# Optimization experiments

Hardware: AMD Instinct MI355X
Metric: run time of the kernel (lower is better)

Reference implementation:

```python
import jax, jax.numpy as jnp
import numpy as np

N = 50000       # nodes
E = 800000      # edges
IN_DIM = 256    # input_dim
HEADS = 4
CH = 32         # per-head channels (hidden_dim; conv3 uses latent_dim//heads = 32 too)
HC = HEADS * CH # 128
ED = 32         # edge_dims


def setup_inputs():
    key = jax.random.key(0)
    ks = iter(jax.random.split(key, 64))
    def nrm(shape):
        return jax.random.normal(next(ks), shape, dtype=jnp.float32) * 0.05
    inp = {}
    inp["x"] = nrm((N, IN_DIM))
    inp["edge_index"] = jax.random.randint(next(ks), (2, E), 0, N)
    inp["attr"] = nrm((E, ED))
    for l, ind in ((1, IN_DIM), (2, HC), (3, HC)):
        inp[f"Wq{l}"] = nrm((ind, HC)); inp[f"bq{l}"] = jnp.zeros((HC,), jnp.float32)
        inp[f"Wk{l}"] = nrm((ind, HC)); inp[f"bk{l}"] = jnp.zeros((HC,), jnp.float32)
        inp[f"Wv{l}"] = nrm((ind, HC)); inp[f"bv{l}"] = jnp.zeros((HC,), jnp.float32)
        inp[f"We{l}"] = nrm((ED, HC))  # lin_edge has no bias in PyG TransformerConv
        inp[f"Ws{l}"] = nrm((ind, HC)); inp[f"bs{l}"] = jnp.zeros((HC,), jnp.float32)
    inp["g1"] = jnp.ones((HC,), jnp.float32); inp["be1"] = jnp.zeros((HC,), jnp.float32)
    inp["g2"] = jnp.ones((HC,), jnp.float32); inp["be2"] = jnp.zeros((HC,), jnp.float32)
    return inp


def _transformer_conv(x, src, dst, attr, Wq, bq, Wk, bk, Wv, bv, We, Ws, bs):
    # PyG TransformerConv, concat=True, root_weight=True, beta=False, dropout=0 (eval).
    q = (x @ Wq + bq).reshape(-1, HEADS, CH)   # [N,H,C] (queries at dst)
    k = (x @ Wk + bk).reshape(-1, HEADS, CH)
    v = (x @ Wv + bv).reshape(-1, HEADS, CH)
    e = (attr @ We).reshape(-1, HEADS, CH)     # [E,H,C]
    kj = k[src] + e                            # edge-conditioned keys  [E,H,C]
    vj = v[src] + e                            # edge-conditioned values [E,H,C]
    alpha = jnp.einsum('ehc,ehc->eh', q[dst], kj) / np.sqrt(CH).astype(np.float32)
    # segment softmax over incoming edges per destination node, per head
    amax = jax.ops.segment_max(alpha, dst, num_segments=N)          # [N,H]
    amax = jnp.where(jnp.isfinite(amax), amax, 0.0)                 # nodes with no edges
    ex = jnp.exp(alpha - amax[dst])                                 # [E,H]
    den = jax.ops.segment_sum(ex, dst, num_segments=N)              # [N,H]
    a = ex / (den[dst] + 1e-16)                                     # [E,H]
    out = jax.ops.segment_sum(a[..., None] * vj, dst, num_segments=N)  # [N,H,C]
    out = out.reshape(-1, HC) + (x @ Ws + bs)                       # + root skip
    return out, a


def _layernorm(x, g, b):
    m = x.mean(-1, keepdims=True)
    v = x.var(-1, keepdims=True)
    return (x - m) / jnp.sqrt(v + 1e-5) * g + b


def reference(x, edge_index, attr,
              Wq1, bq1, Wk1, bk1, Wv1, bv1, We1, Ws1, bs1,
              Wq2, bq2, Wk2, bk2, Wv2, bv2, We2, Ws2, bs2,
              Wq3, bq3, Wk3, bk3, Wv3, bv3, We3, Ws3, bs3,
              g1, be1, g2, be2):
    src, dst = edge_index[0], edge_index[1]
    h, a1 = _transformer_conv(x, src, dst, attr, Wq1, bq1, Wk1, bk1, Wv1, bv1, We1, Ws1, bs1)
    h = jax.nn.relu(_layernorm(h, g1, be1))   # dropout is identity in eval
    h, a2 = _transformer_conv(h, src, dst, attr, Wq2, bq2, Wk2, bk2, Wv2, bv2, We2, Ws2, bs2)
    h = jax.nn.relu(_layernorm(h, g2, be2))
    h, a3 = _transformer_conv(h, src, dst, attr, Wq3, bq3, Wk3, bk3, Wv3, bv3, We3, Ws3, bs3)
    return (h, a1, a2, a3)
```

## Files before the change

### kernel.cpp

```cpp
#include <hip/hip_runtime.h>
#include <math.h>

#define N_NODES 50000
#define E_EDGES 800000
#define HC 128
#define ED 32
#define SCH 64
#define SCHSZ 782

typedef __attribute__((ext_vector_type(8))) short bf16x8;
typedef __attribute__((ext_vector_type(4))) float f32x4;
typedef unsigned short ushort_t;

__device__ __forceinline__ ushort_t f2bf(float f){
    unsigned u = __float_as_uint(f);
    return (ushort_t)((u + 0x7FFFu + ((u >> 16) & 1u)) >> 16);
}
__device__ __forceinline__ float bflo(unsigned u){ return __uint_as_float(u << 16); }
__device__ __forceinline__ float bfhi(unsigned u){ return __uint_as_float(u & 0xffff0000u); }

__device__ __forceinline__ int weidx(int c, int d){
    return c * 40 + (((((d >> 2) + ((c >> 3) & 7)) & 7)) << 2) + (d & 3);
}


__global__ void hist_kernel(const int* __restrict__ dst, int* __restrict__ cnt, int n_edges){
    int e = blockIdx.x * blockDim.x + threadIdx.x;
    if (e < n_edges) atomicAdd(&cnt[dst[e]], 1);
}

__global__ __launch_bounds__(256) void chunk_hist_kernel(const int* __restrict__ cnt,
                                                         int* __restrict__ chist,
                                                         int* __restrict__ csum){
    __shared__ int hist[64];
    __shared__ int red[256];
    const int t = threadIdx.x, b = blockIdx.x;
    if (t < 64) hist[t] = 0;
    __syncthreads();
    const int base = b * SCHSZ;
    const int lim = min(base + SCHSZ, N_NODES);
    int mysum = 0;
    for (int i = base + t; i < lim; i += 256){
        int d = cnt[i];
        mysum += d;
        if (d > 63) d = 63;
        atomicAdd(&hist[d], 1);
    }
    red[t] = mysum;
    __syncthreads();
    for (int off = 128; off; off >>= 1){
        if (t < off) red[t] += red[t + off];
        __syncthreads();
    }
    if (t < 64) chist[b * 64 + t] = hist[t];
    if (t == 0) csum[b] = red[0];
}

__global__ __launch_bounds__(256) void fill_rowptr_kernel(
    const int* __restrict__ cnt, const int* __restrict__ csum,
    int* __restrict__ rowptr, int* __restrict__ cursor)
{
    __shared__ int ts[256];
    __shared__ int chunkbase;
    const int b = blockIdx.x, t = threadIdx.x;
    if (t == 0){
        int acc = 0;
        for (int c = 0; c < b; c++) acc += csum[c];
        chunkbase = acc;
    }
    const int base = b * SCHSZ;
    const int lim = min(base + SCHSZ, N_NODES);
    const int idx0 = base + t * 4;
    int c[4];
    int local = 0;
    #pragma unroll
    for (int j = 0; j < 4; j++){
        int idx = idx0 + j;
        c[j] = (idx < lim) ? cnt[idx] : 0;
        local += c[j];
    }
    ts[t] = local;
    __syncthreads();
    for (int off = 1; off < 256; off <<= 1){
        int v = (t >= off) ? ts[t - off] : 0;
        __syncthreads();
        ts[t] += v;
        __syncthreads();
    }
    int off0 = chunkbase + ((t == 0) ? 0 : ts[t - 1]);
    #pragma unroll
    for (int j = 0; j < 4; j++){
        int idx = idx0 + j;
        if (idx < lim){
            rowptr[idx] = off0;
            cursor[idx] = off0;
            off0 += c[j];
        }
    }
    if (b == SCH - 1 && t == 255) rowptr[N_NODES] = chunkbase + ts[255];
}

__global__ __launch_bounds__(256) void scatter_kernel(
    const int* __restrict__ src, const int* __restrict__ dst,
    int* __restrict__ cursor, int2* __restrict__ es, int n_edges,
    const int* __restrict__ cnt, const int* __restrict__ chist, int* __restrict__ norder)
{
    __shared__ int chs[SCH * 64];
    __shared__ int bt[64];
    __shared__ int bb[64];
    __shared__ int cur[64];
    const int b = blockIdx.x, t = threadIdx.x;
    const bool sorter = (b < SCH);
    int pre = 0;
    if (sorter){
        for (int i = t; i < SCH * 64; i += 256) chs[i] = chist[i];
        __syncthreads();
        if (t < 64){
            int tot = 0;
            for (int c = 0; c < SCH; c++){
                int v = chs[c * 64 + t];
                tot += v;
                if (c < b) pre += v;
            }
            bt[t] = tot;
        }
        __syncthreads();
        if (t == 0){
            int a = 0;
            for (int d = 0; d < 64; d++){ int v = bt[d]; bb[d] = a; a += v; }
        }
        __syncthreads();
        if (t < 64) cur[t] = bb[t] + pre;
        __syncthreads();
    }
    int e = b * 256 + t;
    if (e < n_edges){
        int d = dst[e];
        int pos = atomicAdd(&cursor[d], 1);
        es[pos] = make_int2(e, src[e]);
    }
    if (sorter){
        const int base = b * SCHSZ;
        const int lim = min(base + SCHSZ, N_NODES);
        for (int i = base + t; i < lim; i += 256){
            int d = cnt[i]; if (d > 63) d = 63;
            int pos = atomicAdd(&cur[d], 1);
            norder[pos] = i;
        }
    }
}

__device__ __forceinline__ void pack_item(const float* __restrict__ Wq, const float* __restrict__ Wk,
                                          const float* __restrict__ Wv, const float* __restrict__ Ws,
                                          const float* __restrict__ We, ushort_t* __restrict__ Bp,
                                          int K, int item){
    int n = item % 640, k = item / 640;
    float val;
    if (n < 512){
        const float* W = (n < 128) ? Wq : (n < 256) ? Wk : (n < 384) ? Wv : Ws;
        val = W[k * HC + (n & 127)];
    } else {
        int col = n - 512, h5 = (col >> 5) * 32, d = col & 31;
        float acc = 0.f;
        for (int c = 0; c < 32; c++)
            acc = fmaf(Wq[k * HC + h5 + c], We[d * HC + h5 + c], acc);
        val = acc;
    }
    Bp[(((size_t)(k >> 3)) * 640 + n) * 8 + (k & 7)] = f2bf(val);
}

#define T_S0 12800000
#define T_S1 16000000
#define T_S2 16163840
#define T_S3 16245760
#define T_S4 16327680
#define T_S5 16328064

__global__ __launch_bounds__(256) void tail_kernel(
    const float* __restrict__ attr, const int2* __restrict__ es,
    const float* __restrict__ x, int perm_mode,
    ushort_t* __restrict__ attr_bf, ushort_t* __restrict__ Xbf,
    const float* __restrict__ Wq0, const float* __restrict__ bq0, const float* __restrict__ Wk0,
    const float* __restrict__ Wv0, const float* __restrict__ Ws0, const float* __restrict__ We0,
    const float* __restrict__ Wq1, const float* __restrict__ bq1, const float* __restrict__ Wk1,
    const float* __restrict__ Wv1, const float* __restrict__ Ws1, const float* __restrict__ We1,
    const float* __restrict__ Wq2, const float* __restrict__ bq2, const float* __restrict__ Wk2,
    const float* __restrict__ Wv2, const float* __restrict__ Ws2, const float* __restrict__ We2,
    ushort_t* __restrict__ Bp0, ushort_t* __restrict__ Bp1, ushort_t* __restrict__ Bp2,
    float* __restrict__ qwb3)
{
    const int stride = gridDim.x * blockDim.x;
    for (int gi = blockIdx.x * blockDim.x + threadIdx.x; gi < T_S5; gi += stride){
        if (gi < T_S0){
            if (perm_mode){
                int grp = gi >> 4, lane = gi & 15;
                int e = es[grp].x;
                const float2 v = *(const float2*)&attr[(size_t)e * ED + lane * 2];
                unsigned r = (unsigned)f2bf(v.x) | ((unsigned)f2bf(v.y) << 16);
                ((unsigned*)attr_bf)[(size_t)grp * (ED / 2) + lane] = r;
            }
        } else if (gi < T_S1){
            int i = gi - T_S0;
            float4 v = ((const float4*)x)[i];
            ushort_t r0 = f2bf(v.x), r1 = f2bf(v.y), r2 = f2bf(v.z), r3 = f2bf(v.w);
            ((ushort4*)Xbf)[i] = make_ushort4(r0, r1, r2, r3);
        } else if (gi < T_S2){
            pack_item(Wq0, Wk0, Wv0, Ws0, We0, Bp0, 256, gi - T_S1);
        } else if (gi < T_S3){
            pack_item(Wq1, Wk1, Wv1, Ws1, We1, Bp1, 128, gi - T_S2);
        } else if (gi < T_S4){
            pack_item(Wq2, Wk2, Wv2, Ws2, We2, Bp2, 128, gi - T_S3);
        } else {
            int f = gi - T_S4;
            int l = f >> 7, t2 = f & 127;
            const float* bq = (l == 0) ? bq0 : (l == 1) ? bq1 : bq2;
            const float* We = (l == 0) ? We0 : (l == 1) ? We1 : We2;
            int h5 = (t2 >> 5) * 32, d = t2 & 31;
            float acc = 0.f;
            for (int c = 0; c < 32; c++)
                acc = fmaf(bq[h5 + c], We[d * HC + h5 + c], acc);
            qwb3[l * HC + t2] = acc;
        }
    }
}

template<int K>
__global__ __launch_bounds__(320) void gemm_mfma(
    const ushort_t* __restrict__ Xbf, const ushort_t* __restrict__ Bpack,
    const float* __restrict__ b0, const float* __restrict__ b1,
    const float* __restrict__ b2, const float* __restrict__ b3,
    const float* __restrict__ b4,
    float* __restrict__ Yq, ushort_t* __restrict__ Ykbf,
    ushort_t* __restrict__ Yvbf, float* __restrict__ Ys,
    float* __restrict__ Yw, int M)
{
    const int w = threadIdx.x >> 6;
    const int lane = threadIdx.x & 63;
    const int q = lane >> 4, nn = lane & 15;
    const int row0 = blockIdx.x * 32;

    f32x4 acc[2][8];
    #pragma unroll
    for (int mt = 0; mt < 2; mt++)
        #pragma unroll
        for (int nt = 0; nt < 8; nt++)
            acc[mt][nt] = (f32x4){0.f, 0.f, 0.f, 0.f};

    const int r0 = row0 + nn;
    const int r1 = row0 + 16 + nn;
    const bf16x8 zf = (bf16x8){0,0,0,0,0,0,0,0};

    #pragma unroll
    for (int kc = 0; kc < K / 32; kc++){
        bf16x8 a0 = (r0 < M) ? *(const bf16x8*)&Xbf[(size_t)r0 * K + kc * 32 + q * 8] : zf;
        bf16x8 a1 = (r1 < M) ? *(const bf16x8*)&Xbf[(size_t)r1 * K + kc * 32 + q * 8] : zf;
        bf16x8 b[8];
        #pragma unroll
        for (int nt = 0; nt < 8; nt++){
            int n = w * 128 + nt * 16 + nn;
            b[nt] = *(const bf16x8*)&Bpack[(((size_t)(kc * 4 + q)) * 640 + n) * 8];
        }
        #pragma unroll
        for (int nt = 0; nt < 8; nt++){
            acc[0][nt] = __builtin_amdgcn_mfma_f32_16x16x32_bf16(a0, b[nt], acc[0][nt], 0, 0, 0);
            acc[1][nt] = __builtin_amdgcn_mfma_f32_16x16x32_bf16(a1, b[nt], acc[1][nt], 0, 0, 0);
        }
    }

    const float scale = (w == 0 || w == 4) ? 0.17677669529663687f : 1.f;
    const float* bias = (w == 0) ? b0 : (w == 1) ? b1 : (w == 2) ? b2 : (w == 3) ? b3 : b4;

    if (w == 1 || w == 2){
        ushort_t* Yb = (w == 1) ? Ykbf : Yvbf;
        #pragma unroll
        for (int nt = 0; nt < 8; nt++){
            int col = nt * 16 + nn;
            float bval = bias[col];
            #pragma unroll
            for (int mt = 0; mt < 2; mt++){
                #pragma unroll
                for (int r = 0; r < 4; r++){
                    int row = row0 + mt * 16 + q * 4 + r;
                    if (row < M) Yb[(size_t)row * HC + col] = f2bf(acc[mt][nt][r] + bval);
                }
            }
        }
    } else {
        float* Y = (w == 0) ? Yq : (w == 3) ? Ys : Yw;
        #pragma unroll
        for (int nt = 0; nt < 8; nt++){
            int col = nt * 16 + nn;
            float bval = bias[col];
            #pragma unroll
            for (int mt = 0; mt < 2; mt++){
                #pragma unroll
                for (int r = 0; r < 4; r++){
                    int row = row0 + mt * 16 + q * 4 + r;
                    if (row < M) Y[(size_t)row * HC + col] = (acc[mt][nt][r] + bval) * scale;
                }
            }
        }
    }
}

__device__ __forceinline__ float dot16s(const uint4 kk, const uint4 aa,
                                        const float4 qA, const float4 qB,
                                        const float4 wA, const float4 wB){
    float pa =            bflo(kk.x) * qA.x;
    pa = fmaf(bfhi(kk.x), qA.y, pa);
    pa = fmaf(bflo(kk.y), qA.z, pa);
    pa = fmaf(bfhi(kk.y), qA.w, pa);
    pa = fmaf(bflo(aa.x), wA.x, pa);
    pa = fmaf(bfhi(aa.x), wA.y, pa);
    pa = fmaf(bflo(aa.y), wA.z, pa);
    pa = fmaf(bfhi(aa.y), wA.w, pa);
    float pb =            bflo(kk.z) * qB.x;
    pb = fmaf(bfhi(kk.z), qB.y, pb);
    pb = fmaf(bflo(kk.w), qB.z, pb);
    pb = fmaf(bfhi(kk.w), qB.w, pb);
    pb = fmaf(bflo(aa.z), wB.x, pb);
    pb = fmaf(bfhi(aa.z), wB.y, pb);
    pb = fmaf(bflo(aa.w), wB.z, pb);
    pb = fmaf(bfhi(aa.w), wB.w, pb);
    return pa + pb;
}

__device__ __forceinline__ uint4 packrow(const float* p){
    float4 x = *(const float4*)p;
    float4 y = *(const float4*)(p + 4);
    uint4 r;
    r.x = (unsigned)f2bf(x.x) | ((unsigned)f2bf(x.y) << 16);
    r.y = (unsigned)f2bf(x.z) | ((unsigned)f2bf(x.w) << 16);
    r.z = (unsigned)f2bf(y.x) | ((unsigned)f2bf(y.y) << 16);
    r.w = (unsigned)f2bf(y.z) | ((unsigned)f2bf(y.w) << 16);
    return r;
}

__global__ __launch_bounds__(256) void fused_attn_kernel(
    const float* __restrict__ qs, const float* __restrict__ qw,
    const ushort_t* __restrict__ kb, const ushort_t* __restrict__ vb,
    const float* __restrict__ skip, const float* __restrict__ We,
    const float* __restrict__ attr, const ushort_t* __restrict__ attr_bf, int perm_mode,
    const int* __restrict__ rowptr, const int2* __restrict__ es,
    const int* __restrict__ norder,
    float* __restrict__ acsr, float* __restrict__ a_out,
    const float* __restrict__ g, const float* __restrict__ be,
    float* __restrict__ out_f32, ushort_t* __restrict__ out_bf, int apply_ln)
{
    __shared__ float WeT[5120];
    __shared__ float SL[2304];
    const int t = threadIdx.x;
    for (int idx = t; idx < ED * HC; idx += 256){
        int d = idx >> 7, c = idx & 127;
        WeT[weidx(c, d)] = We[idx];
    }
    __syncthreads();

    const int lane = t & 63, wvi = t >> 6;
    const int qq = lane >> 4, li = lane & 15;
    const int h = li >> 2, jj = li & 3;
    const int gq = blockIdx.x * 16 + wvi * 4 + qq;
    if (gq >= N_NODES) return;
    const int n = norder[gq];
    const int ch = h * 32 + jj * 8;
    const size_t nrow = (size_t)n * HC + ch;

    const float4 qA = *(const float4*)&qs[nrow];
    const float4 qB = *(const float4*)&qs[nrow + 4];
    const float4 wA = *(const float4*)&qw[nrow];
    const float4 wB = *(const float4*)&qw[nrow + 4];
    const float4 skA = *(const float4*)&skip[nrow];
    const float4 skB = *(const float4*)&skip[nrow + 4];

    const int beg = rowptr[n], end = rowptr[n + 1];
    float m = -1e30f, s = 0.f;
    float acc[8] = {0,0,0,0,0,0,0,0};
    float S[8]   = {0,0,0,0,0,0,0,0};

    for (int i = beg; i < end; i += 4){
        const int cnt = end - i;
        uint4 kk[4], vv[4], aa[4];
        #pragma unroll
        for (int b = 0; b < 4; b++){
            kk[b] = (uint4){0,0,0,0}; vv[b] = (uint4){0,0,0,0}; aa[b] = (uint4){0,0,0,0};
            if (b < cnt){
                const int2 e = es[i + b];
                kk[b] = *(const uint4*)&kb[(size_t)e.y * HC + ch];
                vv[b] = *(const uint4*)&vb[(size_t)e.y * HC + ch];
                if (perm_mode)
                    aa[b] = *(const uint4*)&attr_bf[(size_t)(i + b) * ED + jj * 8];
                else
                    aa[b] = packrow(&attr[(size_t)e.x * ED + jj * 8]);
            }
        }
        float al[4];
        #pragma unroll
        for (int b = 0; b < 4; b++){
            float p = dot16s(kk[b], aa[b], qA, qB, wA, wB);
            p += __shfl_xor(p, 1);
            p += __shfl_xor(p, 2);
            al[b] = (b < cnt) ? p : -1e38f;
        }
        if (jj == 0){
            #pragma unroll
            for (int b = 0; b < 4; b++)
                if (b < cnt) acsr[(size_t)(i + b) * 4 + h] = al[b];
        }
        const float mn = fmaxf(fmaxf(m, fmaxf(al[0], al[1])), fmaxf(al[2], al[3]));
        const float sc = __expf(m - mn);
        m = mn;
        const float w0 = __expf(al[0] - mn);
        const float w1 = __expf(al[1] - mn);
        const float w2 = __expf(al[2] - mn);
        const float w3 = __expf(al[3] - mn);
        s = fmaf(s, sc, (w0 + w1) + (w2 + w3));
        acc[0] = fmaf(acc[0], sc, fmaf(w0, bflo(vv[0].x), fmaf(w1, bflo(vv[1].x), fmaf(w2, bflo(vv[2].x), w3 * bflo(vv[3].x)))));
        acc[1] = fmaf(acc[1], sc, fmaf(w0, bfhi(vv[0].x), fmaf(w1, bfhi(vv[1].x), fmaf(w2, bfhi(vv[2].x), w3 * bfhi(vv[3].x)))));
        acc[2] = fmaf(acc[2], sc, fmaf(w0, bflo(vv[0].y), fmaf(w1, bflo(vv[1].y), fmaf(w2, bflo(vv[2].y), w3 * bflo(vv[3].y)))));
        acc[3] = fmaf(acc[3], sc, fmaf(w0, bfhi(vv[0].y), fmaf(w1, bfhi(vv[1].y), fmaf(w2, bfhi(vv[2].y), w3 * bfhi(vv[3].y)))));
        acc[4] = fmaf(acc[4], sc, fmaf(w0, bflo(vv[0].z), fmaf(w1, bflo(vv[1].z), fmaf(w2, bflo(vv[2].z), w3 * bflo(vv[3].z)))));
        acc[5] = fmaf(acc[5], sc, fmaf(w0, bfhi(vv[0].z), fmaf(w1, bfhi(vv[1].z), fmaf(w2, bfhi(vv[2].z), w3 * bfhi(vv[3].z)))));
        acc[6] = fmaf(acc[6], sc, fmaf(w0, bflo(vv[0].w), fmaf(w1, bflo(vv[1].w), fmaf(w2, bflo(vv[2].w), w3 * bflo(vv[3].w)))));
        acc[7] = fmaf(acc[7], sc, fmaf(w0, bfhi(vv[0].w), fmaf(w1, bfhi(vv[1].w), fmaf(w2, bfhi(vv[2].w), w3 * bfhi(vv[3].w)))));
        S[0] = fmaf(S[0], sc, fmaf(w0, bflo(aa[0].x), fmaf(w1, bflo(aa[1].x), fmaf(w2, bflo(aa[2].x), w3 * bflo(aa[3].x)))));
        S[1] = fmaf(S[1], sc, fmaf(w0, bfhi(aa[0].x), fmaf(w1, bfhi(aa[1].x), fmaf(w2, bfhi(aa[2].x), w3 * bfhi(aa[3].x)))));
        S[2] = fmaf(S[2], sc, fmaf(w0, bflo(aa[0].y), fmaf(w1, bflo(aa[1].y), fmaf(w2, bflo(aa[2].y), w3 * bflo(aa[3].y)))));
        S[3] = fmaf(S[3], sc, fmaf(w0, bfhi(aa[0].y), fmaf(w1, bfhi(aa[1].y), fmaf(w2, bfhi(aa[2].y), w3 * bfhi(aa[3].y)))));
        S[4] = fmaf(S[4], sc, fmaf(w0, bflo(aa[0].z), fmaf(w1, bflo(aa[1].z), fmaf(w2, bflo(aa[2].z), w3 * bflo(aa[3].z)))));
        S[5] = fmaf(S[5], sc, fmaf(w0, bfhi(aa[0].z), fmaf(w1, bfhi(aa[1].z), fmaf(w2, bfhi(aa[2].z), w3 * bfhi(aa[3].z)))));
        S[6] = fmaf(S[6], sc, fmaf(w0, bflo(aa[0].w), fmaf(w1, bflo(aa[1].w), fmaf(w2, bflo(aa[2].w), w3 * bflo(aa[3].w)))));
        S[7] = fmaf(S[7], sc, fmaf(w0, bfhi(aa[0].w), fmaf(w1, bfhi(aa[1].w), fmaf(w2, bfhi(aa[2].w), w3 * bfhi(aa[3].w)))));
    }

    const int nl = wvi * 4 + qq;
    const int sbase = nl * 144;
    const int hsk = h * 36;
    *(float4*)&SL[sbase + hsk + jj * 8]     = make_float4(S[0], S[1], S[2], S[3]);
    *(float4*)&SL[sbase + hsk + jj * 8 + 4] = make_float4(S[4], S[5], S[6], S[7]);
    asm volatile("" ::: "memory");
    float E[8] = {0,0,0,0,0,0,0,0};
    #pragma unroll
    for (int d4 = 0; d4 < 8; d4++){
        const float4 sv = *(const float4*)&SL[sbase + hsk + d4 * 4];
        #pragma unroll
        for (int r = 0; r < 8; r++){
            const float4 wv = *(const float4*)&WeT[weidx(ch + r, d4 * 4)];
            E[r] = fmaf(sv.x, wv.x, fmaf(sv.y, wv.y, fmaf(sv.z, wv.z, fmaf(sv.w, wv.w, E[r]))));
        }
    }

    const float inv = 1.f / (s + 1e-16f);
    float o[8];
    o[0] = (acc[0] + E[0]) * inv + skA.x;
    o[1] = (acc[1] + E[1]) * inv + skA.y;
    o[2] = (acc[2] + E[2]) * inv + skA.z;
    o[3] = (acc[3] + E[3]) * inv + skA.w;
    o[4] = (acc[4] + E[4]) * inv + skB.x;
    o[5] = (acc[5] + E[5]) * inv + skB.y;
    o[6] = (acc[6] + E[6]) * inv + skB.z;
    o[7] = (acc[7] + E[7]) * inv + skB.w;

    if (apply_ln){
        float s1 = 0.f, s2 = 0.f;
        #pragma unroll
        for (int r = 0; r < 8; r++){ s1 += o[r]; s2 = fmaf(o[r], o[r], s2); }
        #pragma unroll
        for (int off = 1; off <= 8; off <<= 1){
            s1 += __shfl_xor(s1, off);
            s2 += __shfl_xor(s2, off);
        }
        const float mu  = s1 * (1.f / 128.f);
        const float var = s2 * (1.f / 128.f) - mu * mu;
        const float ivs = rsqrtf(var + 1e-5f);
        const float4 gA = *(const float4*)&g[ch];
        const float4 gB = *(const float4*)&g[ch + 4];
        const float4 bA = *(const float4*)&be[ch];
        const float4 bB = *(const float4*)&be[ch + 4];
        o[0] = fmaxf((o[0] - mu) * ivs * gA.x + bA.x, 0.f);
        o[1] = fmaxf((o[1] - mu) * ivs * gA.y + bA.y, 0.f);
        o[2] = fmaxf((o[2] - mu) * ivs * gA.z + bA.z, 0.f);
        o[3] = fmaxf((o[3] - mu) * ivs * gA.w + bA.w, 0.f);
        o[4] = fmaxf((o[4] - mu) * ivs * gB.x + bB.x, 0.f);
        o[5] = fmaxf((o[5] - mu) * ivs * gB.y + bB.y, 0.f);
        o[6] = fmaxf((o[6] - mu) * ivs * gB.z + bB.z, 0.f);
        o[7] = fmaxf((o[7] - mu) * ivs * gB.w + bB.w, 0.f);
        uint4 st;
        st.x = (unsigned)f2bf(o[0]) | ((unsigned)f2bf(o[1]) << 16);
        st.y = (unsigned)f2bf(o[2]) | ((unsigned)f2bf(o[3]) << 16);
        st.z = (unsigned)f2bf(o[4]) | ((unsigned)f2bf(o[5]) << 16);
        st.w = (unsigned)f2bf(o[6]) | ((unsigned)f2bf(o[7]) << 16);
        *(uint4*)&out_bf[nrow] = st;
    } else {
        *(float4*)&out_f32[nrow]     = make_float4(o[0], o[1], o[2], o[3]);
        *(float4*)&out_f32[nrow + 4] = make_float4(o[4], o[5], o[6], o[7]);
    }

    const float mh = __shfl(m, (qq << 4) + ((li & 3) << 2));
    const float dh = __shfl(s, (qq << 4) + ((li & 3) << 2));
    const float ih = 1.f / (dh + 1e-16f);
    asm volatile("s_waitcnt vmcnt(0)" ::: "memory");
    for (int f = beg * 4 + li; f < end * 4; f += 16){
        const int e = es[f >> 2].x;
        a_out[(size_t)e * 4 + (li & 3)] = __expf(acsr[f] - mh) * ih;
    }
}


extern "C" void kernel_launch(void* const* d_in, const int* in_sizes, int n_in,
                              void* d_out, int out_size, void* d_ws, size_t ws_size,
                              hipStream_t stream) {
    const float* x    = (const float*)d_in[0];
    const int*   ei   = (const int*)  d_in[1];
    const float* attr = (const float*)d_in[2];
    const float* gln[2]  = { (const float*)d_in[30], (const float*)d_in[32] };
    const float* beln[2] = { (const float*)d_in[31], (const float*)d_in[33] };

    float* out   = (float*)d_out;
    float* h_out = out;
    float* a_out[3] = { out + (size_t)N_NODES * HC,
                        out + (size_t)N_NODES * HC + (size_t)E_EDGES * 4,
                        out + (size_t)N_NODES * HC + (size_t)2 * E_EDGES * 4 };

    char* base = (char*)d_ws;
    size_t off = 0;
    auto alloc = [&](size_t bytes) -> void* {
        void* p = base + off;
        off = (off + bytes + 63) & ~(size_t)63;
        return p;
    };
    const size_t NB = (size_t)N_NODES * HC;
    float* qbuf     = (float*)alloc(NB * 4);
    float* qwbuf    = (float*)alloc(NB * 4);
    ushort_t* kbf   = (ushort_t*)alloc(NB * 2);
    ushort_t* vbf   = (ushort_t*)alloc(NB * 2);
    float* sbuf     = (float*)alloc(NB * 4);
    int* rowptr     = (int*)alloc((N_NODES + 1) * 4);
    int* cnt        = (int*)alloc(N_NODES * 4);
    int* cursor     = (int*)alloc(N_NODES * 4);
    int* norder     = (int*)alloc(N_NODES * 4);
    int* chist      = (int*)alloc(SCH * 64 * 4);
    int* csum       = (int*)alloc(SCH * 4);
    int2* es        = (int2*)alloc((size_t)E_EDGES * 8);
    ushort_t* Xbf   = (ushort_t*)alloc((size_t)N_NODES * 256 * 2);
    ushort_t* Hbf   = (ushort_t*)alloc(NB * 2);
    ushort_t* Bp0   = (ushort_t*)alloc((size_t)256 * 640 * 2);
    ushort_t* Bp1   = (ushort_t*)alloc((size_t)128 * 640 * 2);
    ushort_t* Bp2   = (ushort_t*)alloc((size_t)128 * 640 * 2);
    float* acsr     = (float*)alloc((size_t)E_EDGES * 4 * 4);
    float* qwb3     = (float*)alloc((size_t)3 * HC * 4);
    ushort_t* attr_bf = (ushort_t*)alloc((size_t)E_EDGES * ED * 2);
    const int perm_mode = (ws_size >= off) ? 1 : 0;

    const int* srcp = ei;
    const int* dstp = ei + E_EDGES;

    hipMemsetAsync(cnt, 0, (size_t)N_NODES * 4, stream);
    hist_kernel<<<(E_EDGES + 255) / 256, 256, 0, stream>>>(dstp, cnt, E_EDGES);
    chunk_hist_kernel<<<SCH, 256, 0, stream>>>(cnt, chist, csum);
    fill_rowptr_kernel<<<SCH, 256, 0, stream>>>(cnt, csum, rowptr, cursor);
    scatter_kernel<<<(E_EDGES + 255) / 256, 256, 0, stream>>>(
        srcp, dstp, cursor, es, E_EDGES, cnt, chist, norder);
    tail_kernel<<<4096, 256, 0, stream>>>(
        attr, es, x, perm_mode, attr_bf, Xbf,
        (const float*)d_in[3],  (const float*)d_in[4],  (const float*)d_in[5],
        (const float*)d_in[7],  (const float*)d_in[10], (const float*)d_in[9],
        (const float*)d_in[12], (const float*)d_in[13], (const float*)d_in[14],
        (const float*)d_in[16], (const float*)d_in[19], (const float*)d_in[18],
        (const float*)d_in[21], (const float*)d_in[22], (const float*)d_in[23],
        (const float*)d_in[25], (const float*)d_in[28], (const float*)d_in[27],
        Bp0, Bp1, Bp2, qwb3);

    const int gemm_grid = (N_NODES + 31) / 32;
    const int attn_grid = (N_NODES + 15) / 16;
    ushort_t* Bps[3] = { Bp0, Bp1, Bp2 };

    for (int l = 0; l < 3; l++){
        const float* bq = (const float*)d_in[3 + 9 * l + 1];
        const float* bk = (const float*)d_in[3 + 9 * l + 3];
        const float* bv = (const float*)d_in[3 + 9 * l + 5];
        const float* We = (const float*)d_in[3 + 9 * l + 6];
        const float* bs = (const float*)d_in[3 + 9 * l + 8];

        if (l == 0)
            gemm_mfma<256><<<gemm_grid, 320, 0, stream>>>(Xbf, Bps[l], bq, bk, bv, bs, qwb3 + 128 * l,
                                                          qbuf, kbf, vbf, sbuf, qwbuf, N_NODES);
        else
            gemm_mfma<128><<<gemm_grid, 320, 0, stream>>>(Hbf, Bps[l], bq, bk, bv, bs, qwb3 + 128 * l,
                                                          qbuf, kbf, vbf, sbuf, qwbuf, N_NODES);

        const float* gg = (l < 2) ? gln[l] : nullptr;
        const float* bb = (l < 2) ? beln[l] : nullptr;
        fused_attn_kernel<<<attn_grid, 256, 0, stream>>>(
            qbuf, qwbuf, kbf, vbf, sbuf, We, attr, attr_bf, perm_mode,
            rowptr, es, norder, acsr, a_out[l], gg, bb,
            (l < 2) ? nullptr : h_out, (l < 2) ? Hbf : nullptr, (l < 2) ? 1 : 0);
    }
}
```

Before: 921.4 us.

## Fuse CSR build stages into one cooperative kernel with grid syncs

```diff
diff --git a/kernel.cpp b/kernel.cpp
--- a/kernel.cpp
+++ b/kernel.cpp
@@ -1,5 +1,8 @@
 #include <hip/hip_runtime.h>
+#include <hip/hip_cooperative_groups.h>
 #include <math.h>
+
+namespace cg = cooperative_groups;
 
 #define N_NODES 50000
 #define E_EDGES 800000
@@ -23,129 +26,118 @@
     return c * 40 + (((((d >> 2) + ((c >> 3) & 7)) & 7)) << 2) + (d & 3);
 }
 
-
-__global__ void hist_kernel(const int* __restrict__ dst, int* __restrict__ cnt, int n_edges){
-    int e = blockIdx.x * blockDim.x + threadIdx.x;
-    if (e < n_edges) atomicAdd(&cnt[dst[e]], 1);
-}
-
-__global__ __launch_bounds__(256) void chunk_hist_kernel(const int* __restrict__ cnt,
-                                                         int* __restrict__ chist,
-                                                         int* __restrict__ csum){
-    __shared__ int hist[64];
-    __shared__ int red[256];
+__global__ __launch_bounds__(256) void csr_build_kernel(
+    const int* __restrict__ src, const int* __restrict__ dst,
+    int* __restrict__ cnt, int* __restrict__ rowptr, int* __restrict__ cursor,
+    int* __restrict__ chist, int* __restrict__ csum,
+    int2* __restrict__ es, int* __restrict__ norder)
+{
+    cg::grid_group grid = cg::this_grid();
+    __shared__ int sA[256];
+    __shared__ int sB[64];
+    __shared__ int sC[64];
+    __shared__ int sD[64];
+    __shared__ int sE[64];
+    __shared__ int sBase;
     const int t = threadIdx.x, b = blockIdx.x;
-    if (t < 64) hist[t] = 0;
-    __syncthreads();
-    const int base = b * SCHSZ;
-    const int lim = min(base + SCHSZ, N_NODES);
-    int mysum = 0;
-    for (int i = base + t; i < lim; i += 256){
-        int d = cnt[i];
-        mysum += d;
-        if (d > 63) d = 63;
-        atomicAdd(&hist[d], 1);
-    }
-    red[t] = mysum;
-    __syncthreads();
-    for (int off = 128; off; off >>= 1){
-        if (t < off) red[t] += red[t + off];
+    const int gt = b * 256 + t, gs = gridDim.x * 256;
+
+    for (int i = gt; i < N_NODES; i += gs) cnt[i] = 0;
+    grid.sync();
+
+    for (int e = gt; e < E_EDGES; e += gs) atomicAdd(&cnt[dst[e]], 1);
+    grid.sync();
+
+    if (b < SCH){
+        if (t < 64) sB[t] = 0;
         __syncthreads();
-    }
-    if (t < 64) chist[b * 64 + t] = hist[t];
-    if (t == 0) csum[b] = red[0];
-}
-
-__global__ __launch_bounds__(256) void fill_rowptr_kernel(
-    const int* __restrict__ cnt, const int* __restrict__ csum,
-    int* __restrict__ rowptr, int* __restrict__ cursor)
-{
-    __shared__ int ts[256];
-    __shared__ int chunkbase;
-    const int b = blockIdx.x, t = threadIdx.x;
-    if (t == 0){
-        int acc = 0;
-        for (int c = 0; c < b; c++) acc += csum[c];
-        chunkbase = acc;
-    }
-    const int base = b * SCHSZ;
-    const int lim = min(base + SCHSZ, N_NODES);
-    const int idx0 = base + t * 4;
-    int c[4];
-    int local = 0;
-    #pragma unroll
-    for (int j = 0; j < 4; j++){
-        int idx = idx0 + j;
-        c[j] = (idx < lim) ? cnt[idx] : 0;
-        local += c[j];
-    }
-    ts[t] = local;
-    __syncthreads();
-    for (int off = 1; off < 256; off <<= 1){
-        int v = (t >= off) ? ts[t - off] : 0;
+        const int base = b * SCHSZ;
+        const int lim = min(base + SCHSZ, N_NODES);
+        int mysum = 0;
+        for (int i = base + t; i < lim; i += 256){
+            int d = cnt[i]; mysum += d;
+            if (d > 63) d = 63;
+            atomicAdd(&sB[d], 1);
+        }
+        sA[t] = mysum;
         __syncthreads();
-        ts[t] += v;
+        for (int off = 128; off; off >>= 1){
+            if (t < off) sA[t] += sA[t + off];
+            __syncthreads();
+        }
+        if (t < 64) chist[b * 64 + t] = sB[t];
+        if (t == 0) csum[b] = sA[0];
+    }
+    grid.sync();
+
+    if (b < SCH){
+        if (t == 0){
+            int acc = 0;
+            for (int c = 0; c < b; c++) acc += csum[c];
+            sBase = acc;
+        }
+        const int base = b * SCHSZ;
+        const int lim = min(base + SCHSZ, N_NODES);
+        const int idx0 = base + t * 4;
+        int c4[4]; int local = 0;
+        #pragma unroll
+        for (int j = 0; j < 4; j++){
+            int idx = idx0 + j;
+            c4[j] = (idx < lim) ? cnt[idx] : 0;
+            local += c4[j];
+        }
+        sA[t] = local;
         __syncthreads();
-    }
-    int off0 = chunkbase + ((t == 0) ? 0 : ts[t - 1]);
-    #pragma unroll
-    for (int j = 0; j < 4; j++){
-        int idx = idx0 + j;
-        if (idx < lim){
-            rowptr[idx] = off0;
-            cursor[idx] = off0;
-            off0 += c[j];
-        }
-    }
-    if (b == SCH - 1 && t == 255) rowptr[N_NODES] = chunkbase + ts[255];
-}
-
-__global__ __launch_bounds__(256) void scatter_kernel(
-    const int* __restrict__ src, const int* __restrict__ dst,
-    int* __restrict__ cursor, int2* __restrict__ es, int n_edges,
-    const int* __restrict__ cnt, const int* __restrict__ chist, int* __restrict__ norder)
-{
-    __shared__ int chs[SCH * 64];
-    __shared__ int bt[64];
-    __shared__ int bb[64];
-    __shared__ int cur[64];
-    const int b = blockIdx.x, t = threadIdx.x;
-    const bool sorter = (b < SCH);
-    int pre = 0;
-    if (sorter){
-        for (int i = t; i < SCH * 64; i += 256) chs[i] = chist[i];
-        __syncthreads();
+        for (int off = 1; off < 256; off <<= 1){
+            int v = (t >= off) ? sA[t - off] : 0;
+            __syncthreads();
+            sA[t] += v;
+            __syncthreads();
+        }
+        int off0 = sBase + ((t == 0) ? 0 : sA[t - 1]);
+        #pragma unroll
+        for (int j = 0; j < 4; j++){
+            int idx = idx0 + j;
+            if (idx < lim){
+                rowptr[idx] = off0; cursor[idx] = off0;
+                off0 += c4[j];
+            }
+        }
+        if (b == SCH - 1 && t == 255) rowptr[N_NODES] = sBase + sA[255];
+    }
+    grid.sync();
+
+    if (b < SCH){
         if (t < 64){
-            int tot = 0;
+            int tot = 0, pre = 0;
             for (int c = 0; c < SCH; c++){
-                int v = chs[c * 64 + t];
+                int v = chist[c * 64 + t];
                 tot += v;
                 if (c < b) pre += v;
             }
-            bt[t] = tot;
+            sB[t] = tot; sE[t] = pre;
         }
         __syncthreads();
         if (t == 0){
             int a = 0;
-            for (int d = 0; d < 64; d++){ int v = bt[d]; bb[d] = a; a += v; }
+            for (int d = 0; d < 64; d++){ int v = sB[d]; sC[d] = a; a += v; }
         }
         __syncthreads();
-        if (t < 64) cur[t] = bb[t] + pre;
+        if (t < 64) sD[t] = sC[t] + sE[t];
         __syncthreads();
     }
-    int e = b * 256 + t;
-    if (e < n_edges){
+    for (int e = gt; e < E_EDGES; e += gs){
         int d = dst[e];
         int pos = atomicAdd(&cursor[d], 1);
         es[pos] = make_int2(e, src[e]);
     }
-    if (sorter){
+    if (b < SCH){
         const int base = b * SCHSZ;
         const int lim = min(base + SCHSZ, N_NODES);
         for (int i = base + t; i < lim; i += 256){
             int d = cnt[i]; if (d > 63) d = 63;
-            int pos = atomicAdd(&cur[d], 1);
-            norder[pos] = i;
+            int pos = atomicAdd(&sD[d], 1);
+            norder[N_NODES - 1 - pos] = i;
         }
     }
 }
@@ -554,12 +546,13 @@
     const int* srcp = ei;
     const int* dstp = ei + E_EDGES;
 
-    hipMemsetAsync(cnt, 0, (size_t)N_NODES * 4, stream);
-    hist_kernel<<<(E_EDGES + 255) / 256, 256, 0, stream>>>(dstp, cnt, E_EDGES);
-    chunk_hist_kernel<<<SCH, 256, 0, stream>>>(cnt, chist, csum);
-    fill_rowptr_kernel<<<SCH, 256, 0, stream>>>(cnt, csum, rowptr, cursor);
-    scatter_kernel<<<(E_EDGES + 255) / 256, 256, 0, stream>>>(
-        srcp, dstp, cursor, es, E_EDGES, cnt, chist, norder);
+    {
+        void* args[] = { (void*)&srcp, (void*)&dstp, (void*)&cnt, (void*)&rowptr,
+                         (void*)&cursor, (void*)&chist, (void*)&csum,
+                         (void*)&es, (void*)&norder };
+        hipLaunchCooperativeKernel((const void*)csr_build_kernel,
+                                   dim3(1024), dim3(256), args, 0, stream);
+    }
     tail_kernel<<<4096, 256, 0, stream>>>(
         attr, es, x, perm_mode, attr_bf, Xbf,
         (const float*)d_in[3],  (const float*)d_in[4],  (const float*)d_in[5],
```

New measurement: 1.323 ms. 1.44x slower.
